# Kernel tuning notes

Hardware: AMD Instinct MI355X
Metric: run time of the kernel (lower is better)

## Reference

```python
import jax, jax.numpy as jnp
import numpy as np

N_NODES = 50000
N_EDGES = 600000
IN_FEATS = 128
N_HIDDEN = 128
N_CLASSES = 40


def setup_inputs() -> dict:
    key = jax.random.key(0)
    ks = jax.random.split(key, 12)
    feat = jax.random.normal(ks[0], (N_NODES, IN_FEATS), dtype=jnp.float32)
    src = jax.random.randint(ks[1], (N_EDGES,), 0, N_NODES, dtype=jnp.int32)
    dst = jax.random.randint(ks[2], (N_EDGES,), 0, N_NODES, dtype=jnp.int32)
    dims = [(IN_FEATS, N_HIDDEN), (N_HIDDEN, N_HIDDEN), (N_HIDDEN, N_CLASSES)]
    params = {}
    for i, (di, do) in enumerate(dims):
        s = 1.0 / np.sqrt(di)
        params[f"w_self{i}"] = jax.random.uniform(ks[3 + 3 * i], (di, do), jnp.float32, -s, s)
        params[f"w_neigh{i}"] = jax.random.uniform(ks[4 + 3 * i], (di, do), jnp.float32, -s, s)
        params[f"b{i}"] = jnp.zeros((do,), jnp.float32)
    return dict(feat=feat, src=src, dst=dst, **params)


def _sage_layer(h, src, dst, w_self, w_neigh, b):
    # mean aggregation over in-neighbors: msg = h[src], reduce at dst
    msg_sum = jax.ops.segment_sum(h[src], dst, num_segments=N_NODES)  # [N, d]
    deg = jax.ops.segment_sum(jnp.ones((src.shape[0],), h.dtype), dst, num_segments=N_NODES)
    h_neigh = msg_sum / jnp.maximum(deg, 1.0)[:, None]
    # DGL SAGEConv(mean): out = fc_self(h) + fc_neigh(mean_neigh) + bias
    return h @ w_self + h_neigh @ w_neigh + b


def reference(feat, src, dst,
              w_self0, w_neigh0, b0,
              w_self1, w_neigh1, b1,
              w_self2, w_neigh2, b2):
    # dropout p=0.0 -> identity
    h = _sage_layer(feat, src, dst, w_self0, w_neigh0, b0)
    h = jax.nn.relu(h)
    h = _sage_layer(h, src, dst, w_self1, w_neigh1, b1)
    h = jax.nn.relu(h)
    h = _sage_layer(h, src, dst, w_self2, w_neigh2, b2)
    return h
```

## Files before the change

### kernel.cpp

```cpp
#include <hip/hip_runtime.h>

#define N_NODES 50000
#define N_EDGES 600000

typedef short bf16x8 __attribute__((ext_vector_type(8)));
typedef float f32x4  __attribute__((ext_vector_type(4)));
typedef unsigned short u16x8 __attribute__((ext_vector_type(8)));
typedef unsigned short u16x4 __attribute__((ext_vector_type(4)));

__device__ inline ushort rne_bf16(float a) {
    union { float f; unsigned u; } v; v.f = a;
    return (ushort)((v.u + 0x7FFFu + ((v.u >> 16) & 1u)) >> 16);
}
__device__ inline float bf16_to_f32(ushort h) {
    return __uint_as_float((unsigned)h << 16);
}
__device__ inline void split_bf16(float a, ushort& hi, ushort& lo) {
    hi = rne_bf16(a);
    float hv = bf16_to_f32(hi);
    lo = rne_bf16(a - hv);
}


__global__ void count_deg_kernel(const int* __restrict__ dst, int* __restrict__ deg, int ne) {
    int e = blockIdx.x * blockDim.x + threadIdx.x;
    if (e < ne) atomicAdd(&deg[dst[e]], 1);
}

__global__ __launch_bounds__(256) void block_sums_kernel(const int* __restrict__ deg,
                                                         int* __restrict__ bsum, int n) {
    __shared__ int s[256];
    int t = threadIdx.x;
    int i = blockIdx.x * 256 + t;
    s[t] = (i < n) ? deg[i] : 0;
    __syncthreads();
    #pragma unroll
    for (int d = 128; d > 0; d >>= 1) {
        if (t < d) s[t] += s[t + d];
        __syncthreads();
    }
    if (t == 0) bsum[blockIdx.x] = s[0];
}

__global__ __launch_bounds__(256) void scatter_fused_kernel(const int* __restrict__ deg,
                                                            const int* __restrict__ bsum,
                                                            int* __restrict__ off,
                                                            int* __restrict__ cur,
                                                            int n, int nb) {
    __shared__ int s[256];
    int t = threadIdx.x;

    int bv = (t < nb) ? bsum[t] : 0;
    s[t] = bv;
    __syncthreads();
    #pragma unroll
    for (int d = 1; d < 256; d <<= 1) {
        int x = (t >= d) ? s[t - d] : 0;
        __syncthreads();
        s[t] += x;
        __syncthreads();
    }
    int base = (blockIdx.x > 0) ? s[blockIdx.x - 1] : 0;
    if (blockIdx.x == 0 && t == 0) off[n] = s[255];
    __syncthreads();

    int i = blockIdx.x * 256 + t;
    int v = (i < n) ? deg[i] : 0;
    s[t] = v;
    __syncthreads();
    #pragma unroll
    for (int d = 1; d < 256; d <<= 1) {
        int x = (t >= d) ? s[t - d] : 0;
        __syncthreads();
        s[t] += x;
        __syncthreads();
    }
    if (i < n) {
        int excl = s[t] - v + base;
        off[i] = excl;
        cur[i] = excl;
    }
}

__global__ void fill_csr_kernel(const int* __restrict__ src, const int* __restrict__ dst,
                                int* __restrict__ cur, int* __restrict__ ssrc, int ne) {
    int e = blockIdx.x * blockDim.x + threadIdx.x;
    if (e < ne) {
        int p = atomicAdd(&cur[dst[e]], 1);
        ssrc[p] = src[e];
    }
}

__global__ void convert_all_w(const float* __restrict__ ws0, const float* __restrict__ wn0,
                              const float* __restrict__ ws1, const float* __restrict__ wn1,
                              const float* __restrict__ ws2, const float* __restrict__ wn2,
                              ushort* __restrict__ Bth0, ushort* __restrict__ Btl0,
                              ushort* __restrict__ Bth1, ushort* __restrict__ Btl1,
                              ushort* __restrict__ Bth2, ushort* __restrict__ Btl2) {
    int b = blockIdx.x;
    int k = threadIdx.x;
    const float *Ws, *Wn;
    ushort *H, *L;
    int dout, n;
    if (b < 256)      { n = b;       dout = 128; Ws = ws0; Wn = wn0; H = Bth0; L = Btl0; }
    else if (b < 512) { n = b - 256; dout = 128; Ws = ws1; Wn = wn1; H = Bth1; L = Btl1; }
    else              { n = b - 512; dout = 40;  Ws = ws2; Wn = wn2; H = Bth2; L = Btl2; }
    float w = (n < dout) ? Ws[(long)k * dout + n] : Wn[(long)k * dout + (n - dout)];
    ushort hi, lo;
    split_bf16(w, hi, lo);
    H[n * 128 + k] = hi;
    L[n * 128 + k] = lo;
}


#define KDIM 128
#define APAD 136

__device__ inline void load_a16(const float* __restrict__ A, int grow, int M, int seg,
                                float* __restrict__ f) {
    if (grow < M) {
        const float* ap = A + (long)grow * KDIM + seg;
        #pragma unroll
        for (int q = 0; q < 4; ++q) {
            float4 a = *(const float4*)(ap + q * 4);
            f[q * 4 + 0] = a.x; f[q * 4 + 1] = a.y;
            f[q * 4 + 2] = a.z; f[q * 4 + 3] = a.w;
        }
    } else {
        #pragma unroll
        for (int i = 0; i < 16; ++i) f[i] = 0.f;
    }
}

__device__ inline void split_store16(const float* __restrict__ f,
                                     ushort* __restrict__ Ahi, ushort* __restrict__ Alo,
                                     int m, int seg) {
    ushort h[16], l[16];
    #pragma unroll
    for (int i = 0; i < 16; ++i) split_bf16(f[i], h[i], l[i]);
    #pragma unroll
    for (int q = 0; q < 2; ++q) {
        uint4 hw, lw;
        hw.x = (unsigned)h[q*8+0] | ((unsigned)h[q*8+1] << 16);
        hw.y = (unsigned)h[q*8+2] | ((unsigned)h[q*8+3] << 16);
        hw.z = (unsigned)h[q*8+4] | ((unsigned)h[q*8+5] << 16);
        hw.w = (unsigned)h[q*8+6] | ((unsigned)h[q*8+7] << 16);
        lw.x = (unsigned)l[q*8+0] | ((unsigned)l[q*8+1] << 16);
        lw.y = (unsigned)l[q*8+2] | ((unsigned)l[q*8+3] << 16);
        lw.z = (unsigned)l[q*8+4] | ((unsigned)l[q*8+5] << 16);
        lw.w = (unsigned)l[q*8+6] | ((unsigned)l[q*8+7] << 16);
        *(uint4*)&Ahi[m * APAD + seg + q * 8] = hw;
        *(uint4*)&Alo[m * APAD + seg + q * 8] = lw;
    }
}

__global__ __launch_bounds__(256, 3) void gemm_mfma_wide(
    const float* __restrict__ A,
    const ushort* __restrict__ Bth, const ushort* __restrict__ Btl,
    const float* __restrict__ bias,
    float* __restrict__ S, ushort* __restrict__ T, int M)
{
    __shared__ ushort AhiB[2][32 * APAD];
    __shared__ ushort AloB[2][32 * APAD];

    const int tid = threadIdx.x;
    const int wave = tid >> 6;
    const int lane = tid & 63;
    const int lane16 = lane & 15;
    const int quad = lane >> 4;
    const int half = blockIdx.x & 1;
    const int colbase = half * 128 + wave * 32;
    const int ntiles = (M + 31) >> 5;
    const int bstride = gridDim.x >> 1;
    const int m   = tid >> 3;
    const int seg = (tid & 7) * 16;

    bf16x8 Bh[4][2], Bl[4][2];
    #pragma unroll
    for (int c = 0; c < 4; ++c) {
        #pragma unroll
        for (int ct = 0; ct < 2; ++ct) {
            const long boff = (long)(colbase + 16 * ct + lane16) * KDIM + c * 32 + quad * 8;
            Bh[c][ct] = *(const bf16x8*)(Bth + boff);
            Bl[c][ct] = *(const bf16x8*)(Btl + boff);
        }
    }
    f32x4 bv[2] = {};
    if (half == 0) {
        #pragma unroll
        for (int ct = 0; ct < 2; ++ct)
            bv[ct] = *(const f32x4*)(bias + wave * 32 + 16 * ct + quad * 4);
    }

    int rt = blockIdx.x >> 1;
    if (rt >= ntiles) return;

    float fa[16];
    load_a16(A, rt * 32 + m, M, seg, fa);
    split_store16(fa, &AhiB[0][0], &AloB[0][0], m, seg);
    __syncthreads();

    int cur = 0;
    while (true) {
        const int nrt = rt + bstride;
        float fn[16];
        if (nrt < ntiles) load_a16(A, nrt * 32 + m, M, seg, fn);

        const ushort* AH = &AhiB[cur][0];
        const ushort* AL = &AloB[cur][0];

        f32x4 acc[2][2] = {};
        #pragma unroll
        for (int c = 0; c < 4; ++c) {
            const int k0 = c * 32 + quad * 8;
            bf16x8 ah[2], al[2];
            #pragma unroll
            for (int r = 0; r < 2; ++r) {
                const int off = (16 * r + lane16) * APAD + k0;
                ah[r] = *(const bf16x8*)&AH[off];
                al[r] = *(const bf16x8*)&AL[off];
            }
            #pragma unroll
            for (int ct = 0; ct < 2; ++ct) {
                #pragma unroll
                for (int r = 0; r < 2; ++r) {
                    acc[r][ct] = __builtin_amdgcn_mfma_f32_16x16x32_bf16(Bh[c][ct], ah[r], acc[r][ct], 0, 0, 0);
                    acc[r][ct] = __builtin_amdgcn_mfma_f32_16x16x32_bf16(Bl[c][ct], ah[r], acc[r][ct], 0, 0, 0);
                    acc[r][ct] = __builtin_amdgcn_mfma_f32_16x16x32_bf16(Bh[c][ct], al[r], acc[r][ct], 0, 0, 0);
                }
            }
        }

        #pragma unroll
        for (int ct = 0; ct < 2; ++ct) {
            const int colL = wave * 32 + 16 * ct + quad * 4;
            #pragma unroll
            for (int r = 0; r < 2; ++r) {
                const int row = rt * 32 + 16 * r + lane16;
                if (row < M) {
                    if (half == 0) {
                        *(f32x4*)(S + (long)row * 128 + colL) = acc[r][ct] + bv[ct];
                    } else {
                        u16x4 t4;
                        #pragma unroll
                        for (int i = 0; i < 4; ++i) t4[i] = rne_bf16(acc[r][ct][i]);
                        *(u16x4*)(T + (long)row * 128 + colL) = t4;
                    }
                }
            }
        }

        if (nrt >= ntiles) break;
        split_store16(fn, &AhiB[cur ^ 1][0], &AloB[cur ^ 1][0], m, seg);
        __syncthreads();
        cur ^= 1;
        rt = nrt;
    }
}

__global__ __launch_bounds__(256, 2) void gemm_mfma_narrow(
    const float* __restrict__ A,
    const ushort* __restrict__ Bth, const ushort* __restrict__ Btl,
    const float* __restrict__ bias,
    float* __restrict__ S, ushort* __restrict__ T, int M)
{
    __shared__ ushort AhiB[2][32 * APAD];
    __shared__ ushort AloB[2][32 * APAD];

    const int tid = threadIdx.x;
    const int wave = tid >> 6;
    const int lane = tid & 63;
    const int lane16 = lane & 15;
    const int quad = lane >> 4;
    const int rtw = wave & 1;
    const int cg = wave >> 1;
    const int ctbase = cg * 3;
    const int nct = cg ? 2 : 3;
    const int ntiles = (M + 31) >> 5;
    const int m   = tid >> 3;
    const int seg = (tid & 7) * 16;

    bf16x8 Bh[4][3], Bl[4][3];
    #pragma unroll
    for (int c = 0; c < 4; ++c) {
        #pragma unroll
        for (int j = 0; j < 3; ++j) {
            if (j < nct) {
                const long boff = (long)(16 * (ctbase + j) + lane16) * KDIM + c * 32 + quad * 8;
                Bh[c][j] = *(const bf16x8*)(Bth + boff);
                Bl[c][j] = *(const bf16x8*)(Btl + boff);
            }
        }
    }

    int rt = blockIdx.x;
    if (rt >= ntiles) return;

    float fa[16];
    load_a16(A, rt * 32 + m, M, seg, fa);
    split_store16(fa, &AhiB[0][0], &AloB[0][0], m, seg);
    __syncthreads();

    int cur = 0;
    while (true) {
        const int nrt = rt + gridDim.x;
        float fn[16];
        if (nrt < ntiles) load_a16(A, nrt * 32 + m, M, seg, fn);

        const ushort* AH = &AhiB[cur][0];
        const ushort* AL = &AloB[cur][0];

        f32x4 acc[3] = {};
        #pragma unroll
        for (int c = 0; c < 4; ++c) {
            const int off = (rtw * 16 + lane16) * APAD + c * 32 + quad * 8;
            bf16x8 ah = *(const bf16x8*)&AH[off];
            bf16x8 al = *(const bf16x8*)&AL[off];
            #pragma unroll
            for (int j = 0; j < 3; ++j) {
                if (j < nct) {
                    acc[j] = __builtin_amdgcn_mfma_f32_16x16x32_bf16(Bh[c][j], ah, acc[j], 0, 0, 0);
                    acc[j] = __builtin_amdgcn_mfma_f32_16x16x32_bf16(Bl[c][j], ah, acc[j], 0, 0, 0);
                    acc[j] = __builtin_amdgcn_mfma_f32_16x16x32_bf16(Bh[c][j], al, acc[j], 0, 0, 0);
                }
            }
        }

        const int row = rt * 32 + rtw * 16 + lane16;
        #pragma unroll
        for (int j = 0; j < 3; ++j) {
            if (j < nct && row < M) {
                const int col0 = 16 * (ctbase + j) + quad * 4;
                if (col0 < 40) {
                    f32x4 bvv = *(const f32x4*)(bias + col0);
                    *(f32x4*)(S + (long)row * 40 + col0) = acc[j] + bvv;
                } else {
                    u16x4 t4;
                    #pragma unroll
                    for (int i = 0; i < 4; ++i) t4[i] = rne_bf16(acc[j][i]);
                    *(u16x4*)(T + (long)row * 40 + (col0 - 40)) = t4;
                }
            }
        }

        if (nrt >= ntiles) break;
        split_store16(fn, &AhiB[cur ^ 1][0], &AloB[cur ^ 1][0], m, seg);
        __syncthreads();
        cur ^= 1;
        rt = nrt;
    }
}


template <int RELU>
__global__ __launch_bounds__(256) void agg128_kernel(
    const float* __restrict__ S, const ushort* __restrict__ T,
    const int* __restrict__ off, const int* __restrict__ ssrc,
    float* __restrict__ out, int nnodes)
{
    const int node = (blockIdx.x * 256 + threadIdx.x) >> 6;
    if (node >= nnodes) return;
    const int lane = threadIdx.x & 63;
    const int slot = lane >> 4;
    const int col8 = (lane & 15) * 8;

    const int a = off[node];
    const int b = off[node + 1];

    f32x4 acc0a = {0,0,0,0}, acc0b = {0,0,0,0};
    f32x4 acc1a = {0,0,0,0}, acc1b = {0,0,0,0};

    int i = a;
    for (; i + 8 <= b; i += 8) {
        int s0 = ssrc[i + slot];
        int s1 = ssrc[i + 4 + slot];
        u16x8 v0 = *(const u16x8*)(T + (long)s0 * 128 + col8);
        u16x8 v1 = *(const u16x8*)(T + (long)s1 * 128 + col8);
        #pragma unroll
        for (int j = 0; j < 4; ++j) {
            acc0a[j] += bf16_to_f32(v0[j]);
            acc0b[j] += bf16_to_f32(v0[4 + j]);
            acc1a[j] += bf16_to_f32(v1[j]);
            acc1b[j] += bf16_to_f32(v1[4 + j]);
        }
    }
    for (; i < b; i += 4) {
        int e = i + slot;
        if (e < b) {
            int s = ssrc[e];
            u16x8 v = *(const u16x8*)(T + (long)s * 128 + col8);
            #pragma unroll
            for (int j = 0; j < 4; ++j) {
                acc0a[j] += bf16_to_f32(v[j]);
                acc0b[j] += bf16_to_f32(v[4 + j]);
            }
        }
    }
    f32x4 accA = acc0a + acc1a;
    f32x4 accB = acc0b + acc1b;

    #pragma unroll
    for (int m = 16; m <= 32; m <<= 1) {
        #pragma unroll
        for (int j = 0; j < 4; ++j) {
            accA[j] += __shfl_xor((float)accA[j], m);
            accB[j] += __shfl_xor((float)accB[j], m);
        }
    }

    if (slot == 0) {
        int deg = b - a;
        float scale = (deg > 0) ? (1.0f / (float)deg) : 0.f;
        f32x4 sA = *(const f32x4*)(S + (long)node * 128 + col8);
        f32x4 sB = *(const f32x4*)(S + (long)node * 128 + col8 + 4);
        f32x4 rA = sA + accA * scale;
        f32x4 rB = sB + accB * scale;
        if (RELU) {
            #pragma unroll
            for (int j = 0; j < 4; ++j) {
                rA[j] = fmaxf(rA[j], 0.f);
                rB[j] = fmaxf(rB[j], 0.f);
            }
        }
        *(f32x4*)(out + (long)node * 128 + col8) = rA;
        *(f32x4*)(out + (long)node * 128 + col8 + 4) = rB;
    }
}

template <int RELU>
__global__ __launch_bounds__(256) void agg40_kernel(
    const float* __restrict__ S, const ushort* __restrict__ T,
    const int* __restrict__ off, const int* __restrict__ ssrc,
    float* __restrict__ out, int nnodes)
{
    const int node = (blockIdx.x * 256 + threadIdx.x) >> 6;
    if (node >= nnodes) return;
    const int lane = threadIdx.x & 63;
    const bool active = lane < 60;
    const int slot = active ? (lane / 10) : 5;
    const int fi = lane % 10;
    const int fo = fi * 4;

    const int a = off[node];
    const int b = off[node + 1];

    f32x4 acc0 = {0,0,0,0}, acc1 = {0,0,0,0};

    int i = a;
    for (; i + 12 <= b; i += 12) {
        int s0 = ssrc[i + slot];
        int s1 = ssrc[i + 6 + slot];
        u16x4 v0 = *(const u16x4*)(T + (long)s0 * 40 + fo);
        u16x4 v1 = *(const u16x4*)(T + (long)s1 * 40 + fo);
        if (active) {
            #pragma unroll
            for (int j = 0; j < 4; ++j) {
                acc0[j] += bf16_to_f32(v0[j]);
                acc1[j] += bf16_to_f32(v1[j]);
            }
        }
    }
    for (; i < b; i += 6) {
        int e = i + slot;
        if (active && e < b) {
            int s = ssrc[e];
            u16x4 v = *(const u16x4*)(T + (long)s * 40 + fo);
            #pragma unroll
            for (int j = 0; j < 4; ++j) acc0[j] += bf16_to_f32(v[j]);
        }
    }
    f32x4 acc = acc0 + acc1;

    f32x4 tot = acc;
    #pragma unroll
    for (int d = 10; d <= 50; d += 10) {
        int srcl = fi + d;
        #pragma unroll
        for (int j = 0; j < 4; ++j) tot[j] += __shfl((float)acc[j], srcl);
    }

    if (lane < 10) {
        int deg = b - a;
        float scale = (deg > 0) ? (1.0f / (float)deg) : 0.f;
        f32x4 s4 = *(const f32x4*)(S + (long)node * 40 + fo);
        f32x4 r = s4 + tot * scale;
        if (RELU) {
            #pragma unroll
            for (int j = 0; j < 4; ++j) r[j] = fmaxf(r[j], 0.f);
        }
        *(f32x4*)(out + (long)node * 40 + fo) = r;
    }
}


extern "C" void kernel_launch(void* const* d_in, const int* in_sizes, int n_in,
                              void* d_out, int out_size, void* d_ws, size_t ws_size,
                              hipStream_t stream) {
    const float* feat = (const float*)d_in[0];
    const int*   src  = (const int*)d_in[1];
    const int*   dst  = (const int*)d_in[2];
    const float* ws0  = (const float*)d_in[3];
    const float* wn0  = (const float*)d_in[4];
    const float* b0   = (const float*)d_in[5];
    const float* ws1  = (const float*)d_in[6];
    const float* wn1  = (const float*)d_in[7];
    const float* b1   = (const float*)d_in[8];
    const float* ws2  = (const float*)d_in[9];
    const float* wn2  = (const float*)d_in[10];
    const float* b2   = (const float*)d_in[11];

    const int N = N_NODES;
    const int NE = N_EDGES;
    const int NB = (N + 255) / 256;

    char* ws = (char*)d_ws;
    int*    offsets = (int*)(ws + 0);
    int*    cursor  = (int*)(ws + 200704);
    int*    degi    = (int*)(ws + 401408);
    int*    bsum    = (int*)(ws + 601600);
    int*    ssrc    = (int*)(ws + 603648);
    ushort* Bth0 = (ushort*)(ws + 200704);
    ushort* Btl0 = (ushort*)(ws + 266240);
    ushort* Bth1 = (ushort*)(ws + 331776);
    ushort* Btl1 = (ushort*)(ws + 397312);
    ushort* Bth2 = (ushort*)(ws + 462848);
    ushort* Btl2 = (ushort*)(ws + 483328);
    float*  hbuf = (float*)(ws + 3003904);
    float*  sbuf = (float*)(ws + 28603904);
    ushort* tbuf = (ushort*)(ws + 54203904);

    hipMemsetAsync(degi, 0, (size_t)N * sizeof(int), stream);
    count_deg_kernel<<<(NE + 255) / 256, 256, 0, stream>>>(dst, degi, NE);
    block_sums_kernel<<<NB, 256, 0, stream>>>(degi, bsum, N);
    scatter_fused_kernel<<<NB, 256, 0, stream>>>(degi, bsum, offsets, cursor, N, NB);
    fill_csr_kernel<<<(NE + 255) / 256, 256, 0, stream>>>(src, dst, cursor, ssrc, NE);

    convert_all_w<<<592, 128, 0, stream>>>(ws0, wn0, ws1, wn1, ws2, wn2,
                                           Bth0, Btl0, Bth1, Btl1, Bth2, Btl2);

    const int gw = 768;
    const int gn = 512;
    const int ga = (N + 3) / 4;

    gemm_mfma_wide<<<gw, 256, 0, stream>>>(feat, Bth0, Btl0, b0, sbuf, tbuf, N);
    agg128_kernel<1><<<ga, 256, 0, stream>>>(sbuf, tbuf, offsets, ssrc, hbuf, N);

    gemm_mfma_wide<<<gw, 256, 0, stream>>>(hbuf, Bth1, Btl1, b1, sbuf, tbuf, N);
    agg128_kernel<1><<<ga, 256, 0, stream>>>(sbuf, tbuf, offsets, ssrc, hbuf, N);

    gemm_mfma_narrow<<<gn, 256, 0, stream>>>(hbuf, Bth2, Btl2, b2, sbuf, tbuf, N);
    agg40_kernel<0><<<ga, 256, 0, stream>>>(sbuf, tbuf, offsets, ssrc, (float*)d_out, N);
}
```

Measured before the change: 290.0 us.

## Fuse all GraphSAGE stages into one cooperative persistent kernel with grid syncs

Turns each stage into a grid-stride device phase: CSR build (zero, count, block sums, scan, fill), weight bf16 split, and the three GEMM plus aggregation layers. All phases run inside a single cooperative kernel separated by grid.sync, with the grid sized from the occupancy query. The aim is to remove roughly a dozen kernel launches and the gaps between them. In exchange it adds grid-wide barrier cost, and register and shared-memory pressure rises because every phase shares one kernel under launch bounds of 3 blocks per CU. Aggregation now loops over nodes with far fewer blocks. If the cooperative launch fails, it falls back to separate launches.

```diff
diff --git a/kernel.cpp b/kernel.cpp
--- a/kernel.cpp
+++ b/kernel.cpp
@@ -1,7 +1,13 @@
 #include <hip/hip_runtime.h>
+#include <hip/hip_cooperative_groups.h>
+
+namespace cg = cooperative_groups;
 
 #define N_NODES 50000
 #define N_EDGES 600000
+#define NBLK    196
+#define KDIM    128
+#define APAD    136
 
 typedef short bf16x8 __attribute__((ext_vector_type(8)));
 typedef float f32x4  __attribute__((ext_vector_type(4)));
@@ -22,102 +28,112 @@
 }
 
 
-__global__ void count_deg_kernel(const int* __restrict__ dst, int* __restrict__ deg, int ne) {
-    int e = blockIdx.x * blockDim.x + threadIdx.x;
-    if (e < ne) atomicAdd(&deg[dst[e]], 1);
-}
-
-__global__ __launch_bounds__(256) void block_sums_kernel(const int* __restrict__ deg,
-                                                         int* __restrict__ bsum, int n) {
-    __shared__ int s[256];
-    int t = threadIdx.x;
-    int i = blockIdx.x * 256 + t;
-    s[t] = (i < n) ? deg[i] : 0;
-    __syncthreads();
-    #pragma unroll
-    for (int d = 128; d > 0; d >>= 1) {
-        if (t < d) s[t] += s[t + d];
-        __syncthreads();
-    }
-    if (t == 0) bsum[blockIdx.x] = s[0];
-}
-
-__global__ __launch_bounds__(256) void scatter_fused_kernel(const int* __restrict__ deg,
-                                                            const int* __restrict__ bsum,
-                                                            int* __restrict__ off,
-                                                            int* __restrict__ cur,
-                                                            int n, int nb) {
-    __shared__ int s[256];
-    int t = threadIdx.x;
-
-    int bv = (t < nb) ? bsum[t] : 0;
-    s[t] = bv;
-    __syncthreads();
-    #pragma unroll
-    for (int d = 1; d < 256; d <<= 1) {
-        int x = (t >= d) ? s[t - d] : 0;
-        __syncthreads();
-        s[t] += x;
-        __syncthreads();
-    }
-    int base = (blockIdx.x > 0) ? s[blockIdx.x - 1] : 0;
-    if (blockIdx.x == 0 && t == 0) off[n] = s[255];
-    __syncthreads();
-
-    int i = blockIdx.x * 256 + t;
-    int v = (i < n) ? deg[i] : 0;
-    s[t] = v;
-    __syncthreads();
-    #pragma unroll
-    for (int d = 1; d < 256; d <<= 1) {
-        int x = (t >= d) ? s[t - d] : 0;
-        __syncthreads();
-        s[t] += x;
-        __syncthreads();
-    }
-    if (i < n) {
-        int excl = s[t] - v + base;
-        off[i] = excl;
-        cur[i] = excl;
-    }
-}
-
-__global__ void fill_csr_kernel(const int* __restrict__ src, const int* __restrict__ dst,
-                                int* __restrict__ cur, int* __restrict__ ssrc, int ne) {
-    int e = blockIdx.x * blockDim.x + threadIdx.x;
-    if (e < ne) {
+__device__ __forceinline__ void phase_zero(int* __restrict__ degi) {
+    const int gtid = blockIdx.x * 256 + threadIdx.x;
+    const int gsz = gridDim.x * 256;
+    for (int i = gtid; i < N_NODES; i += gsz) degi[i] = 0;
+}
+
+__device__ __forceinline__ void phase_count(const int* __restrict__ dst, int* __restrict__ degi) {
+    const int gtid = blockIdx.x * 256 + threadIdx.x;
+    const int gsz = gridDim.x * 256;
+    for (int e = gtid; e < N_EDGES; e += gsz) atomicAdd(&degi[dst[e]], 1);
+}
+
+__device__ __forceinline__ void phase_bsum(const int* __restrict__ degi, int* __restrict__ bsum,
+                                           int* __restrict__ s) {
+    const int t = threadIdx.x;
+    for (int w = blockIdx.x; w < NBLK; w += gridDim.x) {
+        int i = w * 256 + t;
+        s[t] = (i < N_NODES) ? degi[i] : 0;
+        __syncthreads();
+        #pragma unroll
+        for (int d = 128; d > 0; d >>= 1) {
+            if (t < d) s[t] += s[t + d];
+            __syncthreads();
+        }
+        if (t == 0) bsum[w] = s[0];
+        __syncthreads();
+    }
+}
+
+__device__ __forceinline__ void phase_scan(const int* __restrict__ degi, const int* __restrict__ bsum,
+                                           int* __restrict__ off, int* __restrict__ cur,
+                                           int* __restrict__ s) {
+    const int t = threadIdx.x;
+    for (int w = blockIdx.x; w < NBLK; w += gridDim.x) {
+        int bv = (t < NBLK) ? bsum[t] : 0;
+        s[t] = bv;
+        __syncthreads();
+        #pragma unroll
+        for (int d = 1; d < 256; d <<= 1) {
+            int x = (t >= d) ? s[t - d] : 0;
+            __syncthreads();
+            s[t] += x;
+            __syncthreads();
+        }
+        int base = (w > 0) ? s[w - 1] : 0;
+        if (w == 0 && t == 0) off[N_NODES] = s[255];
+        __syncthreads();
+
+        int i = w * 256 + t;
+        int v = (i < N_NODES) ? degi[i] : 0;
+        s[t] = v;
+        __syncthreads();
+        #pragma unroll
+        for (int d = 1; d < 256; d <<= 1) {
+            int x = (t >= d) ? s[t - d] : 0;
+            __syncthreads();
+            s[t] += x;
+            __syncthreads();
+        }
+        if (i < N_NODES) {
+            int excl = s[t] - v + base;
+            off[i] = excl;
+            cur[i] = excl;
+        }
+        __syncthreads();
+    }
+}
+
+__device__ __forceinline__ void phase_fill(const int* __restrict__ src, const int* __restrict__ dst,
+                                           int* __restrict__ cur, int* __restrict__ ssrcb) {
+    const int gtid = blockIdx.x * 256 + threadIdx.x;
+    const int gsz = gridDim.x * 256;
+    for (int e = gtid; e < N_EDGES; e += gsz) {
         int p = atomicAdd(&cur[dst[e]], 1);
-        ssrc[p] = src[e];
-    }
-}
-
-__global__ void convert_all_w(const float* __restrict__ ws0, const float* __restrict__ wn0,
-                              const float* __restrict__ ws1, const float* __restrict__ wn1,
-                              const float* __restrict__ ws2, const float* __restrict__ wn2,
-                              ushort* __restrict__ Bth0, ushort* __restrict__ Btl0,
-                              ushort* __restrict__ Bth1, ushort* __restrict__ Btl1,
-                              ushort* __restrict__ Bth2, ushort* __restrict__ Btl2) {
-    int b = blockIdx.x;
-    int k = threadIdx.x;
-    const float *Ws, *Wn;
-    ushort *H, *L;
-    int dout, n;
-    if (b < 256)      { n = b;       dout = 128; Ws = ws0; Wn = wn0; H = Bth0; L = Btl0; }
-    else if (b < 512) { n = b - 256; dout = 128; Ws = ws1; Wn = wn1; H = Bth1; L = Btl1; }
-    else              { n = b - 512; dout = 40;  Ws = ws2; Wn = wn2; H = Bth2; L = Btl2; }
-    float w = (n < dout) ? Ws[(long)k * dout + n] : Wn[(long)k * dout + (n - dout)];
-    ushort hi, lo;
-    split_bf16(w, hi, lo);
-    H[n * 128 + k] = hi;
-    L[n * 128 + k] = lo;
-}
-
-
-#define KDIM 128
-#define APAD 136
-
-__device__ inline void load_a16(const float* __restrict__ A, int grow, int M, int seg,
-                                float* __restrict__ f) {
+        ssrcb[p] = src[e];
+    }
+}
+
+__device__ __forceinline__ void phase_convert(
+    const float* __restrict__ ws0, const float* __restrict__ wn0,
+    const float* __restrict__ ws1, const float* __restrict__ wn1,
+    const float* __restrict__ ws2, const float* __restrict__ wn2,
+    ushort* __restrict__ Bth0, ushort* __restrict__ Btl0,
+    ushort* __restrict__ Bth1, ushort* __restrict__ Btl1,
+    ushort* __restrict__ Bth2, ushort* __restrict__ Btl2) {
+    const int gtid = blockIdx.x * 256 + threadIdx.x;
+    const int gsz = gridDim.x * 256;
+    for (int i = gtid; i < 592 * 128; i += gsz) {
+        int bb = i >> 7;
+        int k = i & 127;
+        const float *Ws, *Wn;
+        ushort *H, *L;
+        int dout, n;
+        if (bb < 256)      { n = bb;       dout = 128; Ws = ws0; Wn = wn0; H = Bth0; L = Btl0; }
+        else if (bb < 512) { n = bb - 256; dout = 128; Ws = ws1; Wn = wn1; H = Bth1; L = Btl1; }
+        else               { n = bb - 512; dout = 40;  Ws = ws2; Wn = wn2; H = Bth2; L = Btl2; }
+        float w = (n < dout) ? Ws[(long)k * dout + n] : Wn[(long)k * dout + (n - dout)];
+        ushort hi, lo;
+        split_bf16(w, hi, lo);
+        H[n * 128 + k] = hi;
+        L[n * 128 + k] = lo;
+    }
+}
+
+__device__ __forceinline__ void load_a16(const float* __restrict__ A, int grow, int M, int seg,
+                                         float* __restrict__ f) {
     if (grow < M) {
         const float* ap = A + (long)grow * KDIM + seg;
         #pragma unroll
@@ -132,9 +148,9 @@
     }
 }
 
-__device__ inline void split_store16(const float* __restrict__ f,
-                                     ushort* __restrict__ Ahi, ushort* __restrict__ Alo,
-                                     int m, int seg) {
+__device__ __forceinline__ void split_store16(const float* __restrict__ f,
+                                              ushort* __restrict__ Ahi, ushort* __restrict__ Alo,
+                                              int m, int seg) {
     ushort h[16], l[16];
     #pragma unroll
     for (int i = 0; i < 16; ++i) split_bf16(f[i], h[i], l[i]);
@@ -154,14 +170,14 @@
     }
 }
 
-__global__ __launch_bounds__(256, 3) void gemm_mfma_wide(
+__device__ __forceinline__ void gemm_wide_phase(
     const float* __restrict__ A,
     const ushort* __restrict__ Bth, const ushort* __restrict__ Btl,
     const float* __restrict__ bias,
-    float* __restrict__ S, ushort* __restrict__ T, int M)
+    float* __restrict__ S, ushort* __restrict__ T, char* ldsraw, int M)
 {
-    __shared__ ushort AhiB[2][32 * APAD];
-    __shared__ ushort AloB[2][32 * APAD];
+    ushort* AhiB = (ushort*)ldsraw;
+    ushort* AloB = (ushort*)(ldsraw + 17408);
 
     const int tid = threadIdx.x;
     const int wave = tid >> 6;
@@ -197,7 +213,7 @@
 
     float fa[16];
     load_a16(A, rt * 32 + m, M, seg, fa);
-    split_store16(fa, &AhiB[0][0], &AloB[0][0], m, seg);
+    split_store16(fa, AhiB, AloB, m, seg);
     __syncthreads();
 
     int cur = 0;
@@ -206,8 +222,8 @@
         float fn[16];
         if (nrt < ntiles) load_a16(A, nrt * 32 + m, M, seg, fn);
 
-        const ushort* AH = &AhiB[cur][0];
-        const ushort* AL = &AloB[cur][0];
+        const ushort* AH = AhiB + cur * 4352;
+        const ushort* AL = AloB + cur * 4352;
 
         f32x4 acc[2][2] = {};
         #pragma unroll
@@ -251,21 +267,21 @@
         }
 
         if (nrt >= ntiles) break;
-        split_store16(fn, &AhiB[cur ^ 1][0], &AloB[cur ^ 1][0], m, seg);
+        split_store16(fn, AhiB + (cur ^ 1) * 4352, AloB + (cur ^ 1) * 4352, m, seg);
         __syncthreads();
         cur ^= 1;
         rt = nrt;
     }
 }
 
-__global__ __launch_bounds__(256, 2) void gemm_mfma_narrow(
+__device__ __forceinline__ void gemm_narrow_phase(
     const float* __restrict__ A,
     const ushort* __restrict__ Bth, const ushort* __restrict__ Btl,
     const float* __restrict__ bias,
-    float* __restrict__ S, ushort* __restrict__ T, int M)
+    float* __restrict__ S, ushort* __restrict__ T, char* ldsraw, int M)
 {
-    __shared__ ushort AhiB[2][32 * APAD];
-    __shared__ ushort AloB[2][32 * APAD];
+    ushort* AhiB = (ushort*)ldsraw;
+    ushort* AloB = (ushort*)(ldsraw + 17408);
 
     const int tid = threadIdx.x;
     const int wave = tid >> 6;
@@ -298,7 +314,7 @@
 
     float fa[16];
     load_a16(A, rt * 32 + m, M, seg, fa);
-    split_store16(fa, &AhiB[0][0], &AloB[0][0], m, seg);
+    split_store16(fa, AhiB, AloB, m, seg);
     __syncthreads();
 
     int cur = 0;
@@ -307,8 +323,8 @@
         float fn[16];
         if (nrt < ntiles) load_a16(A, nrt * 32 + m, M, seg, fn);
 
-        const ushort* AH = &AhiB[cur][0];
-        const ushort* AL = &AloB[cur][0];
+        const ushort* AH = AhiB + cur * 4352;
+        const ushort* AL = AloB + cur * 4352;
 
         f32x4 acc[3] = {};
         #pragma unroll
@@ -344,152 +360,247 @@
         }
 
         if (nrt >= ntiles) break;
-        split_store16(fn, &AhiB[cur ^ 1][0], &AloB[cur ^ 1][0], m, seg);
+        split_store16(fn, AhiB + (cur ^ 1) * 4352, AloB + (cur ^ 1) * 4352, m, seg);
         __syncthreads();
         cur ^= 1;
         rt = nrt;
     }
 }
 
-
 template <int RELU>
-__global__ __launch_bounds__(256) void agg128_kernel(
+__device__ __forceinline__ void agg128_phase(
     const float* __restrict__ S, const ushort* __restrict__ T,
-    const int* __restrict__ off, const int* __restrict__ ssrc,
-    float* __restrict__ out, int nnodes)
+    const int* __restrict__ off, const int* __restrict__ ssrcb,
+    float* __restrict__ out)
 {
-    const int node = (blockIdx.x * 256 + threadIdx.x) >> 6;
-    if (node >= nnodes) return;
+    const int wave = threadIdx.x >> 6;
     const int lane = threadIdx.x & 63;
     const int slot = lane >> 4;
     const int col8 = (lane & 15) * 8;
-
-    const int a = off[node];
-    const int b = off[node + 1];
-
-    f32x4 acc0a = {0,0,0,0}, acc0b = {0,0,0,0};
-    f32x4 acc1a = {0,0,0,0}, acc1b = {0,0,0,0};
-
-    int i = a;
-    for (; i + 8 <= b; i += 8) {
-        int s0 = ssrc[i + slot];
-        int s1 = ssrc[i + 4 + slot];
-        u16x8 v0 = *(const u16x8*)(T + (long)s0 * 128 + col8);
-        u16x8 v1 = *(const u16x8*)(T + (long)s1 * 128 + col8);
-        #pragma unroll
-        for (int j = 0; j < 4; ++j) {
-            acc0a[j] += bf16_to_f32(v0[j]);
-            acc0b[j] += bf16_to_f32(v0[4 + j]);
-            acc1a[j] += bf16_to_f32(v1[j]);
-            acc1b[j] += bf16_to_f32(v1[4 + j]);
-        }
-    }
-    for (; i < b; i += 4) {
-        int e = i + slot;
-        if (e < b) {
-            int s = ssrc[e];
-            u16x8 v = *(const u16x8*)(T + (long)s * 128 + col8);
+    const int ngroups = (N_NODES + 3) >> 2;
+
+    for (int g = blockIdx.x; g < ngroups; g += gridDim.x) {
+        const int node = g * 4 + wave;
+        if (node >= N_NODES) continue;
+
+        const int a = off[node];
+        const int b = off[node + 1];
+
+        f32x4 acc0a = {0,0,0,0}, acc0b = {0,0,0,0};
+        f32x4 acc1a = {0,0,0,0}, acc1b = {0,0,0,0};
+
+        int i = a;
+        for (; i + 8 <= b; i += 8) {
+            int s0 = ssrcb[i + slot];
+            int s1 = ssrcb[i + 4 + slot];
+            u16x8 v0 = *(const u16x8*)(T + (long)s0 * 128 + col8);
+            u16x8 v1 = *(const u16x8*)(T + (long)s1 * 128 + col8);
             #pragma unroll
             for (int j = 0; j < 4; ++j) {
-                acc0a[j] += bf16_to_f32(v[j]);
-                acc0b[j] += bf16_to_f32(v[4 + j]);
-            }
-        }
-    }
-    f32x4 accA = acc0a + acc1a;
-    f32x4 accB = acc0b + acc1b;
-
-    #pragma unroll
-    for (int m = 16; m <= 32; m <<= 1) {
-        #pragma unroll
-        for (int j = 0; j < 4; ++j) {
-            accA[j] += __shfl_xor((float)accA[j], m);
-            accB[j] += __shfl_xor((float)accB[j], m);
-        }
-    }
-
-    if (slot == 0) {
-        int deg = b - a;
-        float scale = (deg > 0) ? (1.0f / (float)deg) : 0.f;
-        f32x4 sA = *(const f32x4*)(S + (long)node * 128 + col8);
-        f32x4 sB = *(const f32x4*)(S + (long)node * 128 + col8 + 4);
-        f32x4 rA = sA + accA * scale;
-        f32x4 rB = sB + accB * scale;
-        if (RELU) {
+                acc0a[j] += bf16_to_f32(v0[j]);
+                acc0b[j] += bf16_to_f32(v0[4 + j]);
+                acc1a[j] += bf16_to_f32(v1[j]);
+                acc1b[j] += bf16_to_f32(v1[4 + j]);
+            }
+        }
+        for (; i < b; i += 4) {
+            int e = i + slot;
+            if (e < b) {
+                int s = ssrcb[e];
+                u16x8 v = *(const u16x8*)(T + (long)s * 128 + col8);
+                #pragma unroll
+                for (int j = 0; j < 4; ++j) {
+                    acc0a[j] += bf16_to_f32(v[j]);
+                    acc0b[j] += bf16_to_f32(v[4 + j]);
+                }
+            }
+        }
+        f32x4 accA = acc0a + acc1a;
+        f32x4 accB = acc0b + acc1b;
+
+        #pragma unroll
+        for (int mm = 16; mm <= 32; mm <<= 1) {
             #pragma unroll
             for (int j = 0; j < 4; ++j) {
-                rA[j] = fmaxf(rA[j], 0.f);
-                rB[j] = fmaxf(rB[j], 0.f);
-            }
-        }
-        *(f32x4*)(out + (long)node * 128 + col8) = rA;
-        *(f32x4*)(out + (long)node * 128 + col8 + 4) = rB;
+                accA[j] += __shfl_xor((float)accA[j], mm);
+                accB[j] += __shfl_xor((float)accB[j], mm);
+            }
+        }
+
+        if (slot == 0) {
+            int deg = b - a;
+            float scale = (deg > 0) ? (1.0f / (float)deg) : 0.f;
+            f32x4 sA = *(const f32x4*)(S + (long)node * 128 + col8);
+            f32x4 sB = *(const f32x4*)(S + (long)node * 128 + col8 + 4);
+            f32x4 rA = sA + accA * scale;
+            f32x4 rB = sB + accB * scale;
+            if (RELU) {
+                #pragma unroll
+                for (int j = 0; j < 4; ++j) {
+                    rA[j] = fmaxf(rA[j], 0.f);
+                    rB[j] = fmaxf(rB[j], 0.f);
+                }
+            }
+            *(f32x4*)(out + (long)node * 128 + col8) = rA;
+            *(f32x4*)(out + (long)node * 128 + col8 + 4) = rB;
+        }
     }
 }
 
 template <int RELU>
-__global__ __launch_bounds__(256) void agg40_kernel(
+__device__ __forceinline__ void agg40_phase(
     const float* __restrict__ S, const ushort* __restrict__ T,
-    const int* __restrict__ off, const int* __restrict__ ssrc,
-    float* __restrict__ out, int nnodes)
+    const int* __restrict__ off, const int* __restrict__ ssrcb,
+    float* __restrict__ out)
 {
-    const int node = (blockIdx.x * 256 + threadIdx.x) >> 6;
-    if (node >= nnodes) return;
+    const int wave = threadIdx.x >> 6;
     const int lane = threadIdx.x & 63;
     const bool active = lane < 60;
     const int slot = active ? (lane / 10) : 5;
     const int fi = lane % 10;
     const int fo = fi * 4;
-
-    const int a = off[node];
-    const int b = off[node + 1];
-
-    f32x4 acc0 = {0,0,0,0}, acc1 = {0,0,0,0};
-
-    int i = a;
-    for (; i + 12 <= b; i += 12) {
-        int s0 = ssrc[i + slot];
-        int s1 = ssrc[i + 6 + slot];
-        u16x4 v0 = *(const u16x4*)(T + (long)s0 * 40 + fo);
-        u16x4 v1 = *(const u16x4*)(T + (long)s1 * 40 + fo);
-        if (active) {
+    const int ngroups = (N_NODES + 3) >> 2;
+
+    for (int g = blockIdx.x; g < ngroups; g += gridDim.x) {
+        const int node = g * 4 + wave;
+        if (node >= N_NODES) continue;
+
+        const int a = off[node];
+        const int b = off[node + 1];
+
+        f32x4 acc0 = {0,0,0,0}, acc1 = {0,0,0,0};
+
+        int i = a;
+        for (; i + 12 <= b; i += 12) {
+            int s0 = ssrcb[i + slot];
+            int s1 = ssrcb[i + 6 + slot];
+            u16x4 v0 = *(const u16x4*)(T + (long)s0 * 40 + fo);
+            u16x4 v1 = *(const u16x4*)(T + (long)s1 * 40 + fo);
+            if (active) {
+                #pragma unroll
+                for (int j = 0; j < 4; ++j) {
+                    acc0[j] += bf16_to_f32(v0[j]);
+                    acc1[j] += bf16_to_f32(v1[j]);
+                }
+            }
+        }
+        for (; i < b; i += 6) {
+            int e = i + slot;
+            if (active && e < b) {
+                int s = ssrcb[e];
+                u16x4 v = *(const u16x4*)(T + (long)s * 40 + fo);
+                #pragma unroll
+                for (int j = 0; j < 4; ++j) acc0[j] += bf16_to_f32(v[j]);
+            }
+        }
+        f32x4 acc = acc0 + acc1;
+
+        f32x4 tot = acc;
+        #pragma unroll
+        for (int d = 10; d <= 50; d += 10) {
+            int srcl = fi + d;
             #pragma unroll
-            for (int j = 0; j < 4; ++j) {
-                acc0[j] += bf16_to_f32(v0[j]);
-                acc1[j] += bf16_to_f32(v1[j]);
-            }
-        }
-    }
-    for (; i < b; i += 6) {
-        int e = i + slot;
-        if (active && e < b) {
-            int s = ssrc[e];
-            u16x4 v = *(const u16x4*)(T + (long)s * 40 + fo);
-            #pragma unroll
-            for (int j = 0; j < 4; ++j) acc0[j] += bf16_to_f32(v[j]);
-        }
-    }
-    f32x4 acc = acc0 + acc1;
-
-    f32x4 tot = acc;
-    #pragma unroll
-    for (int d = 10; d <= 50; d += 10) {
-        int srcl = fi + d;
-        #pragma unroll
-        for (int j = 0; j < 4; ++j) tot[j] += __shfl((float)acc[j], srcl);
-    }
-
-    if (lane < 10) {
-        int deg = b - a;
-        float scale = (deg > 0) ? (1.0f / (float)deg) : 0.f;
-        f32x4 s4 = *(const f32x4*)(S + (long)node * 40 + fo);
-        f32x4 r = s4 + tot * scale;
-        if (RELU) {
-            #pragma unroll
-            for (int j = 0; j < 4; ++j) r[j] = fmaxf(r[j], 0.f);
-        }
-        *(f32x4*)(out + (long)node * 40 + fo) = r;
-    }
+            for (int j = 0; j < 4; ++j) tot[j] += __shfl((float)acc[j], srcl);
+        }
+
+        if (lane < 10) {
+            int deg = b - a;
+            float scale = (deg > 0) ? (1.0f / (float)deg) : 0.f;
+            f32x4 s4 = *(const f32x4*)(S + (long)node * 40 + fo);
+            f32x4 r = s4 + tot * scale;
+            if (RELU) {
+                #pragma unroll
+                for (int j = 0; j < 4; ++j) r[j] = fmaxf(r[j], 0.f);
+            }
+            *(f32x4*)(out + (long)node * 40 + fo) = r;
+        }
+    }
+}
+
+
+__global__ __launch_bounds__(256, 3) void mega(
+    const float* feat, const int* src, const int* dst,
+    const float* ws0, const float* wn0, const float* b0,
+    const float* ws1, const float* wn1, const float* b1,
+    const float* ws2, const float* wn2, const float* b2,
+    int* offsets, int* cursor, int* degi, int* bsum, int* ssrcb,
+    ushort* Bth0, ushort* Btl0, ushort* Bth1, ushort* Btl1, ushort* Bth2, ushort* Btl2,
+    float* hbuf, float* sbuf, ushort* tbuf, float* outp)
+{
+    cg::grid_group grid = cg::this_grid();
+    __shared__ __align__(16) char lds[34816];
+    int* si = (int*)lds;
+
+    phase_zero(degi);
+    __threadfence(); grid.sync();
+    phase_count(dst, degi);
+    __threadfence(); grid.sync();
+    phase_bsum(degi, bsum, si);
+    __threadfence(); grid.sync();
+    phase_scan(degi, bsum, offsets, cursor, si);
+    __threadfence(); grid.sync();
+    phase_fill(src, dst, cursor, ssrcb);
+    __threadfence(); grid.sync();
+
+    phase_convert(ws0, wn0, ws1, wn1, ws2, wn2, Bth0, Btl0, Bth1, Btl1, Bth2, Btl2);
+    __threadfence(); grid.sync();
+
+    gemm_wide_phase(feat, Bth0, Btl0, b0, sbuf, tbuf, lds, N_NODES);
+    __threadfence(); grid.sync();
+    agg128_phase<1>(sbuf, tbuf, offsets, ssrcb, hbuf);
+    __threadfence(); grid.sync();
+
+    gemm_wide_phase(hbuf, Bth1, Btl1, b1, sbuf, tbuf, lds, N_NODES);
+    __threadfence(); grid.sync();
+    agg128_phase<1>(sbuf, tbuf, offsets, ssrcb, hbuf);
+    __threadfence(); grid.sync();
+
+    gemm_narrow_phase(hbuf, Bth2, Btl2, b2, sbuf, tbuf, lds, N_NODES);
+    __threadfence(); grid.sync();
+    agg40_phase<0>(sbuf, tbuf, offsets, ssrcb, outp);
+}
+
+
+__global__ __launch_bounds__(256) void k_zero(int* degi) { phase_zero(degi); }
+__global__ __launch_bounds__(256) void k_count(const int* dst, int* degi) { phase_count(dst, degi); }
+__global__ __launch_bounds__(256) void k_bsum(const int* degi, int* bsum) {
+    __shared__ int s[256];
+    phase_bsum(degi, bsum, s);
+}
+__global__ __launch_bounds__(256) void k_scan(const int* degi, const int* bsum, int* off, int* cur) {
+    __shared__ int s[256];
+    phase_scan(degi, bsum, off, cur, s);
+}
+__global__ __launch_bounds__(256) void k_fill(const int* src, const int* dst, int* cur, int* ssrcb) {
+    phase_fill(src, dst, cur, ssrcb);
+}
+__global__ __launch_bounds__(256) void k_convert(
+    const float* ws0, const float* wn0, const float* ws1, const float* wn1,
+    const float* ws2, const float* wn2,
+    ushort* Bth0, ushort* Btl0, ushort* Bth1, ushort* Btl1, ushort* Bth2, ushort* Btl2) {
+    phase_convert(ws0, wn0, ws1, wn1, ws2, wn2, Bth0, Btl0, Bth1, Btl1, Bth2, Btl2);
+}
+__global__ __launch_bounds__(256, 3) void k_gemm_wide(
+    const float* A, const ushort* Bth, const ushort* Btl, const float* bias,
+    float* S, ushort* T, int M) {
+    __shared__ __align__(16) char lds[34816];
+    gemm_wide_phase(A, Bth, Btl, bias, S, T, lds, M);
+}
+__global__ __launch_bounds__(256, 2) void k_gemm_narrow(
+    const float* A, const ushort* Bth, const ushort* Btl, const float* bias,
+    float* S, ushort* T, int M) {
+    __shared__ __align__(16) char lds[34816];
+    gemm_narrow_phase(A, Bth, Btl, bias, S, T, lds, M);
+}
+template <int RELU>
+__global__ __launch_bounds__(256) void k_agg128(
+    const float* S, const ushort* T, const int* off, const int* ssrcb, float* out) {
+    agg128_phase<RELU>(S, T, off, ssrcb, out);
+}
+template <int RELU>
+__global__ __launch_bounds__(256) void k_agg40(
+    const float* S, const ushort* T, const int* off, const int* ssrcb, float* out) {
+    agg40_phase<RELU>(S, T, off, ssrcb, out);
 }
 
 
@@ -509,16 +620,12 @@
     const float* wn2  = (const float*)d_in[10];
     const float* b2   = (const float*)d_in[11];
 
-    const int N = N_NODES;
-    const int NE = N_EDGES;
-    const int NB = (N + 255) / 256;
-
     char* ws = (char*)d_ws;
     int*    offsets = (int*)(ws + 0);
     int*    cursor  = (int*)(ws + 200704);
     int*    degi    = (int*)(ws + 401408);
     int*    bsum    = (int*)(ws + 601600);
-    int*    ssrc    = (int*)(ws + 603648);
+    int*    ssrcb   = (int*)(ws + 603648);
     ushort* Bth0 = (ushort*)(ws + 200704);
     ushort* Btl0 = (ushort*)(ws + 266240);
     ushort* Bth1 = (ushort*)(ws + 331776);
@@ -528,26 +635,41 @@
     float*  hbuf = (float*)(ws + 3003904);
     float*  sbuf = (float*)(ws + 28603904);
     ushort* tbuf = (ushort*)(ws + 54203904);
-
-    hipMemsetAsync(degi, 0, (size_t)N * sizeof(int), stream);
-    count_deg_kernel<<<(NE + 255) / 256, 256, 0, stream>>>(dst, degi, NE);
-    block_sums_kernel<<<NB, 256, 0, stream>>>(degi, bsum, N);
-    scatter_fused_kernel<<<NB, 256, 0, stream>>>(degi, bsum, offsets, cursor, N, NB);
-    fill_csr_kernel<<<(NE + 255) / 256, 256, 0, stream>>>(src, dst, cursor, ssrc, NE);
-
-    convert_all_w<<<592, 128, 0, stream>>>(ws0, wn0, ws1, wn1, ws2, wn2,
+    float*  outp = (float*)d_out;
+
+    int maxb = 0;
+    hipError_t qerr = hipOccupancyMaxActiveBlocksPerMultiprocessor(&maxb, mega, 256, 0);
+    if (qerr != hipSuccess || maxb < 1) maxb = 2;
+    int grid = maxb * 256;
+    if (grid > 1024) grid = 1024;
+    grid &= ~1;
+    if (grid < 2) grid = 2;
+
+    void* args[] = {
+        (void*)&feat, (void*)&src, (void*)&dst,
+        (void*)&ws0, (void*)&wn0, (void*)&b0,
+        (void*)&ws1, (void*)&wn1, (void*)&b1,
+        (void*)&ws2, (void*)&wn2, (void*)&b2,
+        (void*)&offsets, (void*)&cursor, (void*)&degi, (void*)&bsum, (void*)&ssrcb,
+        (void*)&Bth0, (void*)&Btl0, (void*)&Bth1, (void*)&Btl1, (void*)&Bth2, (void*)&Btl2,
+        (void*)&hbuf, (void*)&sbuf, (void*)&tbuf, (void*)&outp
+    };
+
+    hipError_t err = hipLaunchCooperativeKernel(mega, dim3(grid), dim3(256), args, 0, stream);
+
+    if (err != hipSuccess) {
+        k_zero<<<768, 256, 0, stream>>>(degi);
+        k_count<<<768, 256, 0, stream>>>(dst, degi);
+        k_bsum<<<NBLK, 256, 0, stream>>>(degi, bsum);
+        k_scan<<<NBLK, 256, 0, stream>>>(degi, bsum, offsets, cursor);
+        k_fill<<<768, 256, 0, stream>>>(src, dst, cursor, ssrcb);
+        k_convert<<<592, 256, 0, stream>>>(ws0, wn0, ws1, wn1, ws2, wn2,
                                            Bth0, Btl0, Bth1, Btl1, Bth2, Btl2);
-
-    const int gw = 768;
-    const int gn = 512;
-    const int ga = (N + 3) / 4;
-
-    gemm_mfma_wide<<<gw, 256, 0, stream>>>(feat, Bth0, Btl0, b0, sbuf, tbuf, N);
-    agg128_kernel<1><<<ga, 256, 0, stream>>>(sbuf, tbuf, offsets, ssrc, hbuf, N);
-
-    gemm_mfma_wide<<<gw, 256, 0, stream>>>(hbuf, Bth1, Btl1, b1, sbuf, tbuf, N);
-    agg128_kernel<1><<<ga, 256, 0, stream>>>(sbuf, tbuf, offsets, ssrc, hbuf, N);
-
-    gemm_mfma_narrow<<<gn, 256, 0, stream>>>(hbuf, Bth2, Btl2, b2, sbuf, tbuf, N);
-    agg40_kernel<0><<<ga, 256, 0, stream>>>(sbuf, tbuf, offsets, ssrc, (float*)d_out, N);
-}
+        k_gemm_wide<<<768, 256, 0, stream>>>(feat, Bth0, Btl0, b0, sbuf, tbuf, N_NODES);
+        k_agg128<1><<<768, 256, 0, stream>>>(sbuf, tbuf, offsets, ssrcb, hbuf);
+        k_gemm_wide<<<768, 256, 0, stream>>>(hbuf, Bth1, Btl1, b1, sbuf, tbuf, N_NODES);
+        k_agg128<1><<<768, 256, 0, stream>>>(sbuf, tbuf, offsets, ssrcb, hbuf);
+        k_gemm_narrow<<<512, 256, 0, stream>>>(hbuf, Bth2, Btl2, b2, sbuf, tbuf, N_NODES);
+        k_agg40<0><<<768, 256, 0, stream>>>(sbuf, tbuf, offsets, ssrcb, outp);
+    }
+}
```

After: 1.122 ms. 3.87x slower.
